# Kernel optimization log

Measured on AMD Instinct MI355X. Metric: run time of the kernel, lower is better.

The kernel has to match this reference:

```python
import jax, jax.numpy as jnp
import numpy as np

N_ZONE, E_ZONE = 100000, 2000000
N_OUT, E_OUT = 50000, 1000000
N_GND, E_GND = 50000, 1000000
HID = 64


def _gcn_conv(x, W, b, edge_index, edge_weight, num_nodes):
    """PyG GCNConv with normalize=True, add_self_loops=True (fill_value=1).
    out[i] = sum_{e: col[e]=i} d^-1/2[row]*w_e*d^-1/2[col] * (xW)[row[e]]
             + d^-1[i]*(xW)[i] + b
    """
    row, col = edge_index[0], edge_index[1]
    ew = edge_weight.reshape(-1)  # [E,1] -> [E]
    # degree includes self-loop weight of 1
    deg = jax.ops.segment_sum(ew, col, num_segments=num_nodes) + 1.0
    dinv = jnp.where(deg > 0, jax.lax.rsqrt(deg), 0.0)
    norm = dinv[row] * ew * dinv[col]  # [E]
    h = x @ W  # [N, HID] transform first (tiny in-dim)
    agg = jax.ops.segment_sum(norm[:, None] * h[row], col, num_segments=num_nodes)
    agg = agg + (dinv * dinv)[:, None] * h  # self-loop term
    return agg + b


def setup_inputs() -> dict:
    key = jax.random.key(0)
    ks = jax.random.split(key, 16)
    inp = {}
    inp["x_zone"] = jax.random.normal(ks[0], (N_ZONE, 2), dtype=jnp.float32)
    inp["x_outdoor"] = jax.random.normal(ks[1], (N_OUT, 3), dtype=jnp.float32)
    inp["x_ground"] = jax.random.normal(ks[2], (N_GND, 1), dtype=jnp.float32)
    inp["edge_index_zone"] = jax.random.randint(ks[3], (2, E_ZONE), 0, N_ZONE, dtype=jnp.int32)
    inp["edge_index_outdoor"] = jax.random.randint(ks[4], (2, E_OUT), 0, N_OUT, dtype=jnp.int32)
    inp["edge_index_ground"] = jax.random.randint(ks[5], (2, E_GND), 0, N_GND, dtype=jnp.int32)
    # learned params: GCN weights/biases + per-edge attribute parameters
    inp["W_zone"] = jax.random.normal(ks[6], (2, HID), dtype=jnp.float32) * 0.5
    inp["W_outdoor"] = jax.random.normal(ks[7], (3, HID), dtype=jnp.float32) * 0.5
    inp["W_ground"] = jax.random.normal(ks[8], (1, HID), dtype=jnp.float32) * 0.5
    inp["b_zone"] = jnp.zeros((HID,), dtype=jnp.float32)
    inp["b_outdoor"] = jnp.zeros((HID,), dtype=jnp.float32)
    inp["b_ground"] = jnp.zeros((HID,), dtype=jnp.float32)
    # positive edge weights so symmetric normalization deg^-1/2 is finite
    inp["edge_attr_zone"] = jax.random.uniform(ks[9], (E_ZONE, 1), dtype=jnp.float32, minval=0.1, maxval=1.0)
    inp["edge_attr_outdoor"] = jax.random.uniform(ks[10], (E_OUT, 1), dtype=jnp.float32, minval=0.1, maxval=1.0)
    inp["edge_attr_ground"] = jax.random.uniform(ks[11], (E_GND, 1), dtype=jnp.float32, minval=0.1, maxval=1.0)
    return inp


def reference(x_zone, x_outdoor, x_ground,
              edge_index_zone, edge_index_outdoor, edge_index_ground,
              W_zone, W_outdoor, W_ground,
              b_zone, b_outdoor, b_ground,
              edge_attr_zone, edge_attr_outdoor, edge_attr_ground):
    z = _gcn_conv(x_zone, W_zone, b_zone, edge_index_zone, edge_attr_zone, N_ZONE)
    o = _gcn_conv(x_outdoor, W_outdoor, b_outdoor, edge_index_outdoor, edge_attr_outdoor, N_OUT)
    g = _gcn_conv(x_ground, W_ground, b_ground, edge_index_ground, edge_attr_ground, N_GND)
    return (jax.nn.relu(z), jax.nn.relu(o), jax.nn.relu(g))
```

## Files before the change

kernel.cpp:

```cpp
#include <hip/hip_runtime.h>

#define N_ZONE 100000
#define E_ZONE 2000000
#define N_OUT  50000
#define E_OUT  1000000
#define N_GND  50000
#define E_GND  1000000
#define HID    64
#define N_TOT   (N_ZONE + N_OUT + N_GND)
#define E_TOTAL (E_ZONE + E_OUT + E_GND)

#define RANGE   2048
#define RSHIFT  11
#define NBZ     49
#define NBO     25
#define NBG     25
#define NBUCKET (NBZ + NBO + NBG)
#define SL      16
#define CAP     49152
#define OUT_PAD_BASE (NBZ * RANGE)
#define GND_PAD_BASE ((NBZ + NBO) * RANGE)
#define PAD_TOT      (NBUCKET * RANGE)

#define CHUNK  4096
#define NCHUNK ((E_TOTAL + CHUNK - 1) / CHUNK)

#define WCUR  0
#define WREC  128
#define WPDEG (WREC + 2 * NBUCKET * CAP)
#define WPSZ  (WPDEG + NBUCKET * SL * RANGE)
#define WPSO  (WPSZ + NBZ * SL * RANGE * 2)
#define WPSG  (WPSO + NBO * SL * RANGE * 3)
#define WDINV (WPSG + NBG * SL * RANGE)
#define WYZ   (WDINV + PAD_TOT)
#define WYO   (WYZ + 2 * N_ZONE)
#define WYG   (WYO + 4 * N_OUT)
#define WUZ   (WYG + N_GND)
#define WUO   (WUZ + 2 * N_ZONE)
#define WUG   (WUO + 4 * N_OUT)
#define WTOT  (WUG + N_GND)
#define FAST_WS_BYTES ((size_t)WTOT * 4)

__global__ void k_bin(const int* __restrict__ eiz, const float* __restrict__ wz,
                      const int* __restrict__ eio, const float* __restrict__ wo,
                      const int* __restrict__ eig, const float* __restrict__ wg,
                      unsigned* __restrict__ cur, uint2* __restrict__ rec) {
    __shared__ unsigned la[CHUNK];
    __shared__ float    lw[CHUNK];
    __shared__ unsigned hist[NBUCKET];
    __shared__ unsigned sbase[NBUCKET + 1];
    __shared__ unsigned gbase[NBUCKET];
    int tid = threadIdx.x;
    for (int b = tid; b < NBUCKET; b += 256) hist[b] = 0;
    __syncthreads();
    int t0 = blockIdx.x * CHUNK;
    unsigned mya[CHUNK / 256], mybk[CHUNK / 256], myr[CHUNK / 256];
    float myw[CHUNK / 256];
#pragma unroll
    for (int i = 0; i < CHUNK / 256; i++) {
        int t = t0 + i * 256 + tid;
        unsigned b = 0xFFFFFFFFu;
        if (t < E_TOTAL) {
            int row, col; float w;
            if (t < E_ZONE) { row = eiz[t]; col = eiz[E_ZONE + t]; w = wz[t]; b = col >> RSHIFT; }
            else if (t < E_ZONE + E_OUT) { int e = t - E_ZONE; row = eio[e]; col = eio[E_OUT + e]; w = wo[e]; b = NBZ + (col >> RSHIFT); }
            else { int e = t - E_ZONE - E_OUT; row = eig[e]; col = eig[E_GND + e]; w = wg[e]; b = NBZ + NBO + (col >> RSHIFT); }
            mya[i] = ((unsigned)(col & (RANGE - 1)) << 17) | (unsigned)row;
            myw[i] = w;
            myr[i] = atomicAdd(&hist[b], 1u);
        }
        mybk[i] = b;
    }
    __syncthreads();
    if (tid == 0) {
        unsigned acc = 0;
        for (int b = 0; b < NBUCKET; b++) { sbase[b] = acc; acc += hist[b]; }
        sbase[NBUCKET] = acc;
    }
    __syncthreads();
    if (tid < NBUCKET)
        gbase[tid] = hist[tid] ? atomicAdd(&cur[tid], hist[tid]) : 0u;
#pragma unroll
    for (int i = 0; i < CHUNK / 256; i++) {
        if (mybk[i] < NBUCKET) {
            unsigned p = sbase[mybk[i]] + myr[i];
            la[p] = mya[i]; lw[p] = myw[i];
        }
    }
    __syncthreads();
    unsigned total = sbase[NBUCKET];
    for (unsigned p = tid; p < total; p += 256) {
        int lo = 0, hi = NBUCKET;
        while (hi - lo > 1) { int mid = (lo + hi) >> 1; if (sbase[mid] <= p) lo = mid; else hi = mid; }
        unsigned idx = (unsigned)lo * CAP + gbase[lo] + (p - sbase[lo]);
        rec[idx] = make_uint2(la[p], __float_as_uint(lw[p]));
    }
}

__global__ void k_degp(const uint2* __restrict__ rec, const unsigned* __restrict__ cur,
                       float* __restrict__ pdeg) {
    __shared__ float deg[RANGE];
    int r = blockIdx.x / SL, sl = blockIdx.x % SL, tid = threadIdx.x;
    for (int i = tid; i < RANGE; i += 256) deg[i] = 0.0f;
    __syncthreads();
    unsigned c = cur[r];
    size_t b0 = (size_t)r * CAP;
    unsigned per = (c + SL - 1) / SL;
    unsigned s0 = sl * per, s1 = s0 + per; if (s1 > c) s1 = c;
    for (unsigned j = s0 + tid; j < s1; j += 256) {
        uint2 q = rec[b0 + j];
        atomicAdd(&deg[q.x >> 17], __uint_as_float(q.y));
    }
    __syncthreads();
    float* o = pdeg + (size_t)blockIdx.x * RANGE;
    for (int i = tid * 4; i < RANGE; i += 1024)
        *(float4*)&o[i] = *(float4*)&deg[i];
}

__global__ void k_dinvy(const float* __restrict__ xz, const float* __restrict__ xo,
                        const float* __restrict__ xg, float* __restrict__ ws) {
    int p = blockIdx.x * blockDim.x + threadIdx.x;
    if (p >= PAD_TOT) return;
    int r = p >> RSHIFT, i = p & (RANGE - 1);
    float d = 1.0f;
#pragma unroll
    for (int sl = 0; sl < SL; sl++)
        d += ws[WPDEG + (size_t)(r * SL + sl) * RANGE + i];
    float di = rsqrtf(d);
    ws[WDINV + p] = di;
    if (p < OUT_PAD_BASE) {
        if (p < N_ZONE) {
            ws[WYZ + 2 * p]     = di * xz[2 * p];
            ws[WYZ + 2 * p + 1] = di * xz[2 * p + 1];
        }
    } else if (p < GND_PAD_BASE) {
        int idx = p - OUT_PAD_BASE;
        if (idx < N_OUT) {
            ws[WYO + 4 * idx]     = di * xo[3 * idx];
            ws[WYO + 4 * idx + 1] = di * xo[3 * idx + 1];
            ws[WYO + 4 * idx + 2] = di * xo[3 * idx + 2];
            ws[WYO + 4 * idx + 3] = 0.0f;
        }
    } else {
        int idx = p - GND_PAD_BASE;
        if (idx < N_GND) ws[WYG + idx] = di * xg[idx];
    }
}

__global__ void k_sp(float* __restrict__ ws) {
    __shared__ __align__(16) float s[RANGE * 3];
    int r = blockIdx.x / SL, sl = blockIdx.x % SL, tid = threadIdx.x;
    const unsigned* cur = (const unsigned*)(ws + WCUR);
    const uint2* rec = (const uint2*)(ws + WREC);
    int ch, rg; size_t yoff, psoff;
    if (r < NBZ)            { ch = 2; rg = r;             yoff = WYZ; psoff = WPSZ; }
    else if (r < NBZ + NBO) { ch = 3; rg = r - NBZ;       yoff = WYO; psoff = WPSO; }
    else                    { ch = 1; rg = r - NBZ - NBO; yoff = WYG; psoff = WPSG; }
    int tot = RANGE * ch;
    for (int i = tid; i < tot; i += 256) s[i] = 0.0f;
    __syncthreads();
    unsigned c = cur[r];
    size_t b0 = (size_t)r * CAP;
    unsigned per = (c + SL - 1) / SL;
    unsigned s0 = sl * per, s1 = s0 + per; if (s1 > c) s1 = c;
    if (ch == 2) {
        const float2* y = (const float2*)(ws + yoff);
        for (unsigned j = s0 + tid; j < s1; j += 256) {
            uint2 q = rec[b0 + j];
            unsigned colr = q.x >> 17, row = q.x & 0x1FFFFu;
            float w = __uint_as_float(q.y);
            float2 yv = y[row];
            atomicAdd(&s[colr * 2],     w * yv.x);
            atomicAdd(&s[colr * 2 + 1], w * yv.y);
        }
    } else if (ch == 3) {
        const float4* y = (const float4*)(ws + yoff);
        for (unsigned j = s0 + tid; j < s1; j += 256) {
            uint2 q = rec[b0 + j];
            unsigned colr = q.x >> 17, row = q.x & 0x1FFFFu;
            float w = __uint_as_float(q.y);
            float4 yv = y[row];
            atomicAdd(&s[colr * 3],     w * yv.x);
            atomicAdd(&s[colr * 3 + 1], w * yv.y);
            atomicAdd(&s[colr * 3 + 2], w * yv.z);
        }
    } else {
        const float* y = ws + yoff;
        for (unsigned j = s0 + tid; j < s1; j += 256) {
            uint2 q = rec[b0 + j];
            atomicAdd(&s[q.x >> 17], __uint_as_float(q.y) * y[q.x & 0x1FFFFu]);
        }
    }
    __syncthreads();
    float* o = ws + psoff + (size_t)(rg * SL + sl) * tot;
    for (int i = tid * 4; i < tot; i += 1024)
        *(float4*)&o[i] = *(float4*)&s[i];
}

__global__ void k_u(float* __restrict__ ws) {
    int p = blockIdx.x * blockDim.x + threadIdx.x;
    if (p >= PAD_TOT) return;
    int r = p >> RSHIFT, i = p & (RANGE - 1);
    float di = ws[WDINV + p];
    if (p < OUT_PAD_BASE) {
        if (p >= N_ZONE) return;
        float s0 = ws[WYZ + 2 * p], s1 = ws[WYZ + 2 * p + 1];
#pragma unroll
        for (int sl = 0; sl < SL; sl++) {
            const float* ps = ws + WPSZ + (size_t)(r * SL + sl) * RANGE * 2;
            s0 += ps[2 * i]; s1 += ps[2 * i + 1];
        }
        ws[WUZ + 2 * p] = di * s0; ws[WUZ + 2 * p + 1] = di * s1;
    } else if (p < GND_PAD_BASE) {
        int idx = p - OUT_PAD_BASE;
        if (idx >= N_OUT) return;
        int rg = r - NBZ;
        float s0 = ws[WYO + 4 * idx], s1 = ws[WYO + 4 * idx + 1], s2 = ws[WYO + 4 * idx + 2];
#pragma unroll
        for (int sl = 0; sl < SL; sl++) {
            const float* ps = ws + WPSO + (size_t)(rg * SL + sl) * RANGE * 3;
            s0 += ps[3 * i]; s1 += ps[3 * i + 1]; s2 += ps[3 * i + 2];
        }
        ws[WUO + 4 * idx] = di * s0; ws[WUO + 4 * idx + 1] = di * s1; ws[WUO + 4 * idx + 2] = di * s2;
    } else {
        int idx = p - GND_PAD_BASE;
        if (idx >= N_GND) return;
        int rg = r - NBZ - NBO;
        float s0 = ws[WYG + idx];
#pragma unroll
        for (int sl = 0; sl < SL; sl++)
            s0 += ws[WPSG + (size_t)(rg * SL + sl) * RANGE + i];
        ws[WUG + idx] = di * s0;
    }
}

__global__ void k_fin2(const float* __restrict__ ws,
                       const float* __restrict__ Wz, const float* __restrict__ bz,
                       const float* __restrict__ Wo, const float* __restrict__ bo,
                       const float* __restrict__ Wg, const float* __restrict__ bg,
                       float* __restrict__ out) {
    int t = blockIdx.x * blockDim.x + threadIdx.x;
    const int TZ4 = N_ZONE * 16, TO4 = TZ4 + N_OUT * 16, TG4 = TO4 + N_GND * 16;
    if (t < TZ4) {
        int i = t >> 4, jb = (t & 15) << 2;
        float u0 = ws[WUZ + 2 * i], u1 = ws[WUZ + 2 * i + 1];
        float4 w0 = *(const float4*)(Wz + jb);
        float4 w1 = *(const float4*)(Wz + HID + jb);
        float4 bv = *(const float4*)(bz + jb);
        float4 o;
        o.x = fmaxf(bv.x + u0 * w0.x + u1 * w1.x, 0.0f);
        o.y = fmaxf(bv.y + u0 * w0.y + u1 * w1.y, 0.0f);
        o.z = fmaxf(bv.z + u0 * w0.z + u1 * w1.z, 0.0f);
        o.w = fmaxf(bv.w + u0 * w0.w + u1 * w1.w, 0.0f);
        *(float4*)(out + i * HID + jb) = o;
    } else if (t < TO4) {
        int q = t - TZ4;
        int i = q >> 4, jb = (q & 15) << 2;
        const float* u = ws + WUO + 4 * i;
        float u0 = u[0], u1 = u[1], u2 = u[2];
        float4 w0 = *(const float4*)(Wo + jb);
        float4 w1 = *(const float4*)(Wo + HID + jb);
        float4 w2 = *(const float4*)(Wo + 2 * HID + jb);
        float4 bv = *(const float4*)(bo + jb);
        float4 o;
        o.x = fmaxf(bv.x + u0 * w0.x + u1 * w1.x + u2 * w2.x, 0.0f);
        o.y = fmaxf(bv.y + u0 * w0.y + u1 * w1.y + u2 * w2.y, 0.0f);
        o.z = fmaxf(bv.z + u0 * w0.z + u1 * w1.z + u2 * w2.z, 0.0f);
        o.w = fmaxf(bv.w + u0 * w0.w + u1 * w1.w + u2 * w2.w, 0.0f);
        *(float4*)(out + N_ZONE * HID + i * HID + jb) = o;
    } else if (t < TG4) {
        int q = t - TO4;
        int i = q >> 4, jb = (q & 15) << 2;
        float u0 = ws[WUG + i];
        float4 w0 = *(const float4*)(Wg + jb);
        float4 bv = *(const float4*)(bg + jb);
        float4 o;
        o.x = fmaxf(bv.x + u0 * w0.x, 0.0f);
        o.y = fmaxf(bv.y + u0 * w0.y, 0.0f);
        o.z = fmaxf(bv.z + u0 * w0.z, 0.0f);
        o.w = fmaxf(bv.w + u0 * w0.w, 0.0f);
        *(float4*)(out + (N_ZONE + N_OUT) * HID + i * HID + jb) = o;
    }
}

#define F_DEG_Z   0
#define F_DEG_O   (N_ZONE)
#define F_DEG_G   (N_ZONE + N_OUT)
#define F_DEG_TOT N_TOT
#define F_S_Z     F_DEG_TOT
#define F_S_O     (F_S_Z + N_ZONE * 2)
#define F_S_G     (F_S_O + N_OUT * 3)
#define F_TOT     (F_S_G + N_GND * 1)

__global__ void f_init(float* __restrict__ ws) {
    int i = blockIdx.x * blockDim.x + threadIdx.x;
    if (i < F_TOT) ws[i] = (i < F_DEG_TOT) ? 1.0f : 0.0f;
}
__global__ void f_deg(const int* __restrict__ eiz, const float* __restrict__ wz,
                      const int* __restrict__ eio, const float* __restrict__ wo,
                      const int* __restrict__ eig, const float* __restrict__ wg,
                      float* __restrict__ ws) {
    int t = blockIdx.x * blockDim.x + threadIdx.x;
    if (t < E_ZONE) atomicAdd(ws + F_DEG_Z + eiz[E_ZONE + t], wz[t]);
    else if (t < E_ZONE + E_OUT) { int e = t - E_ZONE; atomicAdd(ws + F_DEG_O + eio[E_OUT + e], wo[e]); }
    else if (t < E_ZONE + E_OUT + E_GND) { int e = t - E_ZONE - E_OUT; atomicAdd(ws + F_DEG_G + eig[E_GND + e], wg[e]); }
}
__global__ void f_dinv(float* __restrict__ ws) {
    int i = blockIdx.x * blockDim.x + threadIdx.x;
    if (i < F_DEG_TOT) ws[i] = 1.0f / sqrtf(ws[i]);
}
__global__ void f_scatter(const int* __restrict__ eiz, const float* __restrict__ wz, const float* __restrict__ xz,
                          const int* __restrict__ eio, const float* __restrict__ wo, const float* __restrict__ xo,
                          const int* __restrict__ eig, const float* __restrict__ wg, const float* __restrict__ xg,
                          float* __restrict__ ws) {
    int t = blockIdx.x * blockDim.x + threadIdx.x;
    if (t < E_ZONE) {
        int row = eiz[t], col = eiz[E_ZONE + t];
        float n = ws[F_DEG_Z + row] * wz[t] * ws[F_DEG_Z + col];
        atomicAdd(ws + F_S_Z + col * 2 + 0, n * xz[row * 2 + 0]);
        atomicAdd(ws + F_S_Z + col * 2 + 1, n * xz[row * 2 + 1]);
    } else if (t < E_ZONE + E_OUT) {
        int e = t - E_ZONE;
        int row = eio[e], col = eio[E_OUT + e];
        float n = ws[F_DEG_O + row] * wo[e] * ws[F_DEG_O + col];
        atomicAdd(ws + F_S_O + col * 3 + 0, n * xo[row * 3 + 0]);
        atomicAdd(ws + F_S_O + col * 3 + 1, n * xo[row * 3 + 1]);
        atomicAdd(ws + F_S_O + col * 3 + 2, n * xo[row * 3 + 2]);
    } else if (t < E_ZONE + E_OUT + E_GND) {
        int e = t - E_ZONE - E_OUT;
        int row = eig[e], col = eig[E_GND + e];
        float n = ws[F_DEG_G + row] * wg[e] * ws[F_DEG_G + col];
        atomicAdd(ws + F_S_G + col, n * xg[row]);
    }
}
__global__ void f_final(const float* __restrict__ ws,
                        const float* __restrict__ xz, const float* __restrict__ Wz, const float* __restrict__ bz,
                        const float* __restrict__ xo, const float* __restrict__ Wo, const float* __restrict__ bo,
                        const float* __restrict__ xg, const float* __restrict__ Wg, const float* __restrict__ bg,
                        float* __restrict__ out) {
    int t = blockIdx.x * blockDim.x + threadIdx.x;
    const int TZ = N_ZONE * HID, TO = TZ + N_OUT * HID, TG = TO + N_GND * HID;
    if (t < TZ) {
        int i = t >> 6, j = t & 63;
        float di = ws[F_DEG_Z + i], d2 = di * di;
        float t0 = ws[F_S_Z + i * 2 + 0] + d2 * xz[i * 2 + 0];
        float t1 = ws[F_S_Z + i * 2 + 1] + d2 * xz[i * 2 + 1];
        out[t] = fmaxf(bz[j] + t0 * Wz[j] + t1 * Wz[HID + j], 0.0f);
    } else if (t < TO) {
        int u = t - TZ;
        int i = u >> 6, j = u & 63;
        float di = ws[F_DEG_O + i], d2 = di * di;
        float t0 = ws[F_S_O + i * 3 + 0] + d2 * xo[i * 3 + 0];
        float t1 = ws[F_S_O + i * 3 + 1] + d2 * xo[i * 3 + 1];
        float t2 = ws[F_S_O + i * 3 + 2] + d2 * xo[i * 3 + 2];
        out[t] = fmaxf(bo[j] + t0 * Wo[j] + t1 * Wo[HID + j] + t2 * Wo[2 * HID + j], 0.0f);
    } else if (t < TG) {
        int u = t - TO;
        int i = u >> 6, j = u & 63;
        float di = ws[F_DEG_G + i], d2 = di * di;
        float t0 = ws[F_S_G + i] + d2 * xg[i];
        out[t] = fmaxf(bg[j] + t0 * Wg[j], 0.0f);
    }
}

extern "C" void kernel_launch(void* const* d_in, const int* in_sizes, int n_in,
                              void* d_out, int out_size, void* d_ws, size_t ws_size,
                              hipStream_t stream) {
    const float* xz = (const float*)d_in[0];
    const float* xo = (const float*)d_in[1];
    const float* xg = (const float*)d_in[2];
    const int*  eiz = (const int*)d_in[3];
    const int*  eio = (const int*)d_in[4];
    const int*  eig = (const int*)d_in[5];
    const float* Wz = (const float*)d_in[6];
    const float* Wo = (const float*)d_in[7];
    const float* Wg = (const float*)d_in[8];
    const float* bz = (const float*)d_in[9];
    const float* bo = (const float*)d_in[10];
    const float* bg = (const float*)d_in[11];
    const float* wz = (const float*)d_in[12];
    const float* wo = (const float*)d_in[13];
    const float* wg = (const float*)d_in[14];
    float* out = (float*)d_out;
    float* ws  = (float*)d_ws;

    const int B = 256;

    if (ws_size >= FAST_WS_BYTES) {
        unsigned* cur = (unsigned*)(ws + WCUR);
        uint2* rec = (uint2*)(ws + WREC);
        hipMemsetAsync(cur, 0, 128 * 4, stream);
        k_bin<<<NCHUNK, B, 0, stream>>>(eiz, wz, eio, wo, eig, wg, cur, rec);
        k_degp<<<NBUCKET * SL, B, 0, stream>>>(rec, cur, ws + WPDEG);
        k_dinvy<<<(PAD_TOT + B - 1) / B, B, 0, stream>>>(xz, xo, xg, ws);
        k_sp<<<NBUCKET * SL, B, 0, stream>>>(ws);
        k_u<<<(PAD_TOT + B - 1) / B, B, 0, stream>>>(ws);
        k_fin2<<<(N_TOT * HID / 4 + B - 1) / B, B, 0, stream>>>(ws, Wz, bz, Wo, bo, Wg, bg, out);
    } else {
        const int E_TOT = E_TOTAL, OUT_TOT = N_TOT * HID;
        f_init<<<(F_TOT + B - 1) / B, B, 0, stream>>>(ws);
        f_deg<<<(E_TOT + B - 1) / B, B, 0, stream>>>(eiz, wz, eio, wo, eig, wg, ws);
        f_dinv<<<(F_DEG_TOT + B - 1) / B, B, 0, stream>>>(ws);
        f_scatter<<<(E_TOT + B - 1) / B, B, 0, stream>>>(eiz, wz, xz, eio, wo, xo, eig, wg, xg, ws);
        f_final<<<(OUT_TOT + B - 1) / B, B, 0, stream>>>(ws, xz, Wz, bz, xo, Wo, bo, xg, Wg, bg, out);
    }
}
```

Before: 252.7 us.

## Bin edges by destination and source range, stage source features in LDS

Edges are now binned two-dimensionally by destination range and source-row range, 2475 bins with small fixed capacity. Each scatter block loads the matching slice of source features into shared memory, so the per-edge gather reads LDS instead of random global memory. Feature and partial-sum layouts become planar, and the bin kernel uses a parallel scan and a per-record bin tag instead of a serial scan and binary search. The risks are more bins to scan, overflow of the fixed per-bin capacity (1920) if the edge distribution is skewed, and extra window-loading work with two syncs per bin.

```diff
diff --git a/kernel.cpp b/kernel.cpp
--- a/kernel.cpp
+++ b/kernel.cpp
@@ -16,25 +16,35 @@
 #define NBO     25
 #define NBG     25
 #define NBUCKET (NBZ + NBO + NBG)
+#define RGN     25
+#define ZRSH    12
+#define ORSH    11
+#define NBIN    (NBUCKET * RGN)
+#define ZONE_B0 0
+#define OUT_B0  (NBZ * RGN)
+#define GND_B0  ((NBZ + NBO) * RGN)
 #define SL      16
-#define CAP     49152
+#define CAP_RG  1920
 #define OUT_PAD_BASE (NBZ * RANGE)
 #define GND_PAD_BASE ((NBZ + NBO) * RANGE)
 #define PAD_TOT      (NBUCKET * RANGE)
-
-#define CHUNK  4096
+#define OPL     51200
+
+#define CHUNK  3072
+#define EPT    (CHUNK / 256)
+#define BPT    10
 #define NCHUNK ((E_TOTAL + CHUNK - 1) / CHUNK)
 
 #define WCUR  0
-#define WREC  128
-#define WPDEG (WREC + 2 * NBUCKET * CAP)
+#define WREC  2496
+#define WPDEG (WREC + 2 * NBIN * CAP_RG)
 #define WPSZ  (WPDEG + NBUCKET * SL * RANGE)
 #define WPSO  (WPSZ + NBZ * SL * RANGE * 2)
 #define WPSG  (WPSO + NBO * SL * RANGE * 3)
 #define WDINV (WPSG + NBG * SL * RANGE)
 #define WYZ   (WDINV + PAD_TOT)
 #define WYO   (WYZ + 2 * N_ZONE)
-#define WYG   (WYO + 4 * N_OUT)
+#define WYG   (WYO + 3 * OPL)
 #define WUZ   (WYG + N_GND)
 #define WUO   (WUZ + 2 * N_ZONE)
 #define WUG   (WUO + 4 * N_OUT)
@@ -47,24 +57,34 @@
                       unsigned* __restrict__ cur, uint2* __restrict__ rec) {
     __shared__ unsigned la[CHUNK];
     __shared__ float    lw[CHUNK];
-    __shared__ unsigned hist[NBUCKET];
-    __shared__ unsigned sbase[NBUCKET + 1];
-    __shared__ unsigned gbase[NBUCKET];
+    __shared__ unsigned short lbk[CHUNK];
+    __shared__ unsigned hist[NBIN];
+    __shared__ unsigned sbase[NBIN];
+    __shared__ unsigned gbase[NBIN];
+    __shared__ unsigned tsum[256];
+    __shared__ unsigned stot;
     int tid = threadIdx.x;
-    for (int b = tid; b < NBUCKET; b += 256) hist[b] = 0;
+    for (int b = tid; b < NBIN; b += 256) hist[b] = 0;
     __syncthreads();
     int t0 = blockIdx.x * CHUNK;
-    unsigned mya[CHUNK / 256], mybk[CHUNK / 256], myr[CHUNK / 256];
-    float myw[CHUNK / 256];
-#pragma unroll
-    for (int i = 0; i < CHUNK / 256; i++) {
+    unsigned mya[EPT], mybk[EPT], myr[EPT];
+    float myw[EPT];
+#pragma unroll
+    for (int i = 0; i < EPT; i++) {
         int t = t0 + i * 256 + tid;
         unsigned b = 0xFFFFFFFFu;
         if (t < E_TOTAL) {
             int row, col; float w;
-            if (t < E_ZONE) { row = eiz[t]; col = eiz[E_ZONE + t]; w = wz[t]; b = col >> RSHIFT; }
-            else if (t < E_ZONE + E_OUT) { int e = t - E_ZONE; row = eio[e]; col = eio[E_OUT + e]; w = wo[e]; b = NBZ + (col >> RSHIFT); }
-            else { int e = t - E_ZONE - E_OUT; row = eig[e]; col = eig[E_GND + e]; w = wg[e]; b = NBZ + NBO + (col >> RSHIFT); }
+            if (t < E_ZONE) {
+                row = eiz[t]; col = eiz[E_ZONE + t]; w = wz[t];
+                b = ZONE_B0 + (unsigned)(col >> RSHIFT) * RGN + (unsigned)(row >> ZRSH);
+            } else if (t < E_ZONE + E_OUT) {
+                int e = t - E_ZONE; row = eio[e]; col = eio[E_OUT + e]; w = wo[e];
+                b = OUT_B0 + (unsigned)(col >> RSHIFT) * RGN + (unsigned)(row >> ORSH);
+            } else {
+                int e = t - E_ZONE - E_OUT; row = eig[e]; col = eig[E_GND + e]; w = wg[e];
+                b = GND_B0 + (unsigned)(col >> RSHIFT) * RGN + (unsigned)(row >> ORSH);
+            }
             mya[i] = ((unsigned)(col & (RANGE - 1)) << 17) | (unsigned)row;
             myw[i] = w;
             myr[i] = atomicAdd(&hist[b], 1u);
@@ -72,27 +92,46 @@
         mybk[i] = b;
     }
     __syncthreads();
+    {
+        unsigned base = (unsigned)tid * BPT, acc = 0;
+#pragma unroll
+        for (int k = 0; k < BPT; k++) {
+            unsigned b = base + k;
+            if (b < NBIN) acc += hist[b];
+        }
+        tsum[tid] = acc;
+    }
+    __syncthreads();
     if (tid == 0) {
-        unsigned acc = 0;
-        for (int b = 0; b < NBUCKET; b++) { sbase[b] = acc; acc += hist[b]; }
-        sbase[NBUCKET] = acc;
-    }
-    __syncthreads();
-    if (tid < NBUCKET)
-        gbase[tid] = hist[tid] ? atomicAdd(&cur[tid], hist[tid]) : 0u;
-#pragma unroll
-    for (int i = 0; i < CHUNK / 256; i++) {
-        if (mybk[i] < NBUCKET) {
+        unsigned a = 0;
+        for (int i = 0; i < 256; i++) { unsigned v = tsum[i]; tsum[i] = a; a += v; }
+        stot = a;
+    }
+    __syncthreads();
+    {
+        unsigned base = (unsigned)tid * BPT, acc = tsum[tid];
+#pragma unroll
+        for (int k = 0; k < BPT; k++) {
+            unsigned b = base + k;
+            if (b < NBIN) { sbase[b] = acc; acc += hist[b]; }
+        }
+    }
+    for (int b = tid; b < NBIN; b += 256)
+        gbase[b] = hist[b] ? atomicAdd(&cur[b], hist[b]) : 0u;
+    __syncthreads();
+#pragma unroll
+    for (int i = 0; i < EPT; i++) {
+        if (mybk[i] < NBIN) {
             unsigned p = sbase[mybk[i]] + myr[i];
             la[p] = mya[i]; lw[p] = myw[i];
-        }
-    }
-    __syncthreads();
-    unsigned total = sbase[NBUCKET];
+            lbk[p] = (unsigned short)mybk[i];
+        }
+    }
+    __syncthreads();
+    unsigned total = stot;
     for (unsigned p = tid; p < total; p += 256) {
-        int lo = 0, hi = NBUCKET;
-        while (hi - lo > 1) { int mid = (lo + hi) >> 1; if (sbase[mid] <= p) lo = mid; else hi = mid; }
-        unsigned idx = (unsigned)lo * CAP + gbase[lo] + (p - sbase[lo]);
+        unsigned b = lbk[p];
+        unsigned idx = b * CAP_RG + gbase[b] + (p - sbase[b]);
         rec[idx] = make_uint2(la[p], __float_as_uint(lw[p]));
     }
 }
@@ -103,13 +142,30 @@
     int r = blockIdx.x / SL, sl = blockIdx.x % SL, tid = threadIdx.x;
     for (int i = tid; i < RANGE; i += 256) deg[i] = 0.0f;
     __syncthreads();
-    unsigned c = cur[r];
-    size_t b0 = (size_t)r * CAP;
-    unsigned per = (c + SL - 1) / SL;
-    unsigned s0 = sl * per, s1 = s0 + per; if (s1 > c) s1 = c;
-    for (unsigned j = s0 + tid; j < s1; j += 256) {
-        uint2 q = rec[b0 + j];
-        atomicAdd(&deg[q.x >> 17], __uint_as_float(q.y));
+    int bin0;
+    if (r < NBZ)            bin0 = ZONE_B0 + r * RGN;
+    else if (r < NBZ + NBO) bin0 = OUT_B0 + (r - NBZ) * RGN;
+    else                    bin0 = GND_B0 + (r - NBZ - NBO) * RGN;
+#pragma unroll
+    for (int gi = 0; gi < 2; gi++) {
+        int g = sl + gi * SL;
+        if (g >= RGN) break;
+        unsigned bin = bin0 + g;
+        unsigned c = cur[bin];
+        size_t rb = (size_t)bin * CAP_RG;
+        unsigned j = tid;
+        for (; j + 256u * 3 < c; j += 256u * 4) {
+            uint2 q[4];
+#pragma unroll
+            for (int u = 0; u < 4; u++) q[u] = rec[rb + j + 256u * u];
+#pragma unroll
+            for (int u = 0; u < 4; u++)
+                atomicAdd(&deg[(q[u].x >> 17) & (RANGE - 1)], __uint_as_float(q[u].y));
+        }
+        for (; j < c; j += 256u) {
+            uint2 q = rec[rb + j];
+            atomicAdd(&deg[(q.x >> 17) & (RANGE - 1)], __uint_as_float(q.y));
+        }
     }
     __syncthreads();
     float* o = pdeg + (size_t)blockIdx.x * RANGE;
@@ -136,10 +192,9 @@
     } else if (p < GND_PAD_BASE) {
         int idx = p - OUT_PAD_BASE;
         if (idx < N_OUT) {
-            ws[WYO + 4 * idx]     = di * xo[3 * idx];
-            ws[WYO + 4 * idx + 1] = di * xo[3 * idx + 1];
-            ws[WYO + 4 * idx + 2] = di * xo[3 * idx + 2];
-            ws[WYO + 4 * idx + 3] = 0.0f;
+            ws[WYO + idx]           = di * xo[3 * idx];
+            ws[WYO + OPL + idx]     = di * xo[3 * idx + 1];
+            ws[WYO + 2 * OPL + idx] = di * xo[3 * idx + 2];
         }
     } else {
         int idx = p - GND_PAD_BASE;
@@ -148,53 +203,151 @@
 }
 
 __global__ void k_sp(float* __restrict__ ws) {
-    __shared__ __align__(16) float s[RANGE * 3];
+    __shared__ __align__(16) float lds[12288];
     int r = blockIdx.x / SL, sl = blockIdx.x % SL, tid = threadIdx.x;
     const unsigned* cur = (const unsigned*)(ws + WCUR);
     const uint2* rec = (const uint2*)(ws + WREC);
-    int ch, rg; size_t yoff, psoff;
-    if (r < NBZ)            { ch = 2; rg = r;             yoff = WYZ; psoff = WPSZ; }
-    else if (r < NBZ + NBO) { ch = 3; rg = r - NBZ;       yoff = WYO; psoff = WPSO; }
-    else                    { ch = 1; rg = r - NBZ - NBO; yoff = WYG; psoff = WPSG; }
-    int tot = RANGE * ch;
-    for (int i = tid; i < tot; i += 256) s[i] = 0.0f;
-    __syncthreads();
-    unsigned c = cur[r];
-    size_t b0 = (size_t)r * CAP;
-    unsigned per = (c + SL - 1) / SL;
-    unsigned s0 = sl * per, s1 = s0 + per; if (s1 > c) s1 = c;
-    if (ch == 2) {
-        const float2* y = (const float2*)(ws + yoff);
-        for (unsigned j = s0 + tid; j < s1; j += 256) {
-            uint2 q = rec[b0 + j];
-            unsigned colr = q.x >> 17, row = q.x & 0x1FFFFu;
-            float w = __uint_as_float(q.y);
-            float2 yv = y[row];
-            atomicAdd(&s[colr * 2],     w * yv.x);
-            atomicAdd(&s[colr * 2 + 1], w * yv.y);
-        }
-    } else if (ch == 3) {
-        const float4* y = (const float4*)(ws + yoff);
-        for (unsigned j = s0 + tid; j < s1; j += 256) {
-            uint2 q = rec[b0 + j];
-            unsigned colr = q.x >> 17, row = q.x & 0x1FFFFu;
-            float w = __uint_as_float(q.y);
-            float4 yv = y[row];
-            atomicAdd(&s[colr * 3],     w * yv.x);
-            atomicAdd(&s[colr * 3 + 1], w * yv.y);
-            atomicAdd(&s[colr * 3 + 2], w * yv.z);
-        }
+    if (r < NBZ) {
+        float* win = lds;
+        float* s   = lds + 8192;
+        for (int i = tid; i < 4096; i += 256) s[i] = 0.0f;
+        int bin0 = ZONE_B0 + r * RGN;
+#pragma unroll
+        for (int gi = 0; gi < 2; gi++) {
+            int g = sl + gi * SL;
+            if (g >= RGN) break;
+            __syncthreads();
+            int row0 = g << ZRSH;
+            int nw = 2 * (min(4096, N_ZONE - row0));
+            const float4* src = (const float4*)(ws + WYZ + 2 * row0);
+            for (int i = tid; i * 4 < nw; i += 256)
+                ((float4*)win)[i] = src[i];
+            __syncthreads();
+            unsigned bin = bin0 + g;
+            unsigned c = cur[bin];
+            size_t rb = (size_t)bin * CAP_RG;
+            unsigned j = tid;
+            for (; j + 256u * 3 < c; j += 256u * 4) {
+                uint2 q[4];
+#pragma unroll
+                for (int u = 0; u < 4; u++) q[u] = rec[rb + j + 256u * u];
+#pragma unroll
+                for (int u = 0; u < 4; u++) {
+                    unsigned colr = (q[u].x >> 17) & (RANGE - 1);
+                    unsigned loc = q[u].x & 4095u;
+                    float w = __uint_as_float(q[u].y);
+                    float2 yv = *(const float2*)&win[loc * 2];
+                    atomicAdd(&s[colr],        w * yv.x);
+                    atomicAdd(&s[2048 + colr], w * yv.y);
+                }
+            }
+            for (; j < c; j += 256u) {
+                uint2 q = rec[rb + j];
+                unsigned colr = (q.x >> 17) & (RANGE - 1);
+                unsigned loc = q.x & 4095u;
+                float w = __uint_as_float(q.y);
+                float2 yv = *(const float2*)&win[loc * 2];
+                atomicAdd(&s[colr],        w * yv.x);
+                atomicAdd(&s[2048 + colr], w * yv.y);
+            }
+        }
+        __syncthreads();
+        float* o = ws + WPSZ + (size_t)(r * SL + sl) * 4096;
+        for (int i = tid * 4; i < 4096; i += 1024)
+            *(float4*)&o[i] = *(float4*)&s[i];
+    } else if (r < NBZ + NBO) {
+        int rg = r - NBZ;
+        float* win = lds;
+        float* s   = lds + 6144;
+        for (int i = tid; i < 6144; i += 256) s[i] = 0.0f;
+        int bin0 = OUT_B0 + rg * RGN;
+#pragma unroll
+        for (int gi = 0; gi < 2; gi++) {
+            int g = sl + gi * SL;
+            if (g >= RGN) break;
+            __syncthreads();
+            int row0 = g << ORSH;
+            int nv = min(2048, N_OUT - row0);
+#pragma unroll
+            for (int pl = 0; pl < 3; pl++) {
+                const float4* src = (const float4*)(ws + WYO + pl * OPL + row0);
+                for (int i = tid; i * 4 < nv; i += 256)
+                    ((float4*)(win + pl * 2048))[i] = src[i];
+            }
+            __syncthreads();
+            unsigned bin = bin0 + g;
+            unsigned c = cur[bin];
+            size_t rb = (size_t)bin * CAP_RG;
+            unsigned j = tid;
+            for (; j + 256u * 3 < c; j += 256u * 4) {
+                uint2 q[4];
+#pragma unroll
+                for (int u = 0; u < 4; u++) q[u] = rec[rb + j + 256u * u];
+#pragma unroll
+                for (int u = 0; u < 4; u++) {
+                    unsigned colr = (q[u].x >> 17) & (RANGE - 1);
+                    unsigned loc = q[u].x & 2047u;
+                    float w = __uint_as_float(q[u].y);
+                    atomicAdd(&s[colr],        w * win[loc]);
+                    atomicAdd(&s[2048 + colr], w * win[2048 + loc]);
+                    atomicAdd(&s[4096 + colr], w * win[4096 + loc]);
+                }
+            }
+            for (; j < c; j += 256u) {
+                uint2 q = rec[rb + j];
+                unsigned colr = (q.x >> 17) & (RANGE - 1);
+                unsigned loc = q.x & 2047u;
+                float w = __uint_as_float(q.y);
+                atomicAdd(&s[colr],        w * win[loc]);
+                atomicAdd(&s[2048 + colr], w * win[2048 + loc]);
+                atomicAdd(&s[4096 + colr], w * win[4096 + loc]);
+            }
+        }
+        __syncthreads();
+        float* o = ws + WPSO + (size_t)(rg * SL + sl) * 6144;
+        for (int i = tid * 4; i < 6144; i += 1024)
+            *(float4*)&o[i] = *(float4*)&s[i];
     } else {
-        const float* y = ws + yoff;
-        for (unsigned j = s0 + tid; j < s1; j += 256) {
-            uint2 q = rec[b0 + j];
-            atomicAdd(&s[q.x >> 17], __uint_as_float(q.y) * y[q.x & 0x1FFFFu]);
-        }
-    }
-    __syncthreads();
-    float* o = ws + psoff + (size_t)(rg * SL + sl) * tot;
-    for (int i = tid * 4; i < tot; i += 1024)
-        *(float4*)&o[i] = *(float4*)&s[i];
+        int rg = r - NBZ - NBO;
+        float* win = lds;
+        float* s   = lds + 2048;
+        for (int i = tid; i < 2048; i += 256) s[i] = 0.0f;
+        int bin0 = GND_B0 + rg * RGN;
+#pragma unroll
+        for (int gi = 0; gi < 2; gi++) {
+            int g = sl + gi * SL;
+            if (g >= RGN) break;
+            __syncthreads();
+            int row0 = g << ORSH;
+            int nv = min(2048, N_GND - row0);
+            const float4* src = (const float4*)(ws + WYG + row0);
+            for (int i = tid; i * 4 < nv; i += 256)
+                ((float4*)win)[i] = src[i];
+            __syncthreads();
+            unsigned bin = bin0 + g;
+            unsigned c = cur[bin];
+            size_t rb = (size_t)bin * CAP_RG;
+            unsigned j = tid;
+            for (; j + 256u * 3 < c; j += 256u * 4) {
+                uint2 q[4];
+#pragma unroll
+                for (int u = 0; u < 4; u++) q[u] = rec[rb + j + 256u * u];
+#pragma unroll
+                for (int u = 0; u < 4; u++)
+                    atomicAdd(&s[(q[u].x >> 17) & (RANGE - 1)],
+                              __uint_as_float(q[u].y) * win[q[u].x & 2047u]);
+            }
+            for (; j < c; j += 256u) {
+                uint2 q = rec[rb + j];
+                atomicAdd(&s[(q.x >> 17) & (RANGE - 1)],
+                          __uint_as_float(q.y) * win[q.x & 2047u]);
+            }
+        }
+        __syncthreads();
+        float* o = ws + WPSG + (size_t)(rg * SL + sl) * 2048;
+        for (int i = tid * 4; i < 2048; i += 1024)
+            *(float4*)&o[i] = *(float4*)&s[i];
+    }
 }
 
 __global__ void k_u(float* __restrict__ ws) {
@@ -207,19 +360,19 @@
         float s0 = ws[WYZ + 2 * p], s1 = ws[WYZ + 2 * p + 1];
 #pragma unroll
         for (int sl = 0; sl < SL; sl++) {
-            const float* ps = ws + WPSZ + (size_t)(r * SL + sl) * RANGE * 2;
-            s0 += ps[2 * i]; s1 += ps[2 * i + 1];
+            const float* ps = ws + WPSZ + (size_t)(r * SL + sl) * 4096;
+            s0 += ps[i]; s1 += ps[2048 + i];
         }
         ws[WUZ + 2 * p] = di * s0; ws[WUZ + 2 * p + 1] = di * s1;
     } else if (p < GND_PAD_BASE) {
         int idx = p - OUT_PAD_BASE;
         if (idx >= N_OUT) return;
         int rg = r - NBZ;
-        float s0 = ws[WYO + 4 * idx], s1 = ws[WYO + 4 * idx + 1], s2 = ws[WYO + 4 * idx + 2];
+        float s0 = ws[WYO + idx], s1 = ws[WYO + OPL + idx], s2 = ws[WYO + 2 * OPL + idx];
 #pragma unroll
         for (int sl = 0; sl < SL; sl++) {
-            const float* ps = ws + WPSO + (size_t)(rg * SL + sl) * RANGE * 3;
-            s0 += ps[3 * i]; s1 += ps[3 * i + 1]; s2 += ps[3 * i + 2];
+            const float* ps = ws + WPSO + (size_t)(rg * SL + sl) * 6144;
+            s0 += ps[i]; s1 += ps[2048 + i]; s2 += ps[4096 + i];
         }
         ws[WUO + 4 * idx] = di * s0; ws[WUO + 4 * idx + 1] = di * s1; ws[WUO + 4 * idx + 2] = di * s2;
     } else {
@@ -229,7 +382,7 @@
         float s0 = ws[WYG + idx];
 #pragma unroll
         for (int sl = 0; sl < SL; sl++)
-            s0 += ws[WPSG + (size_t)(rg * SL + sl) * RANGE + i];
+            s0 += ws[WPSG + (size_t)(rg * SL + sl) * 2048 + i];
         ws[WUG + idx] = di * s0;
     }
 }
@@ -389,7 +542,7 @@
     if (ws_size >= FAST_WS_BYTES) {
         unsigned* cur = (unsigned*)(ws + WCUR);
         uint2* rec = (uint2*)(ws + WREC);
-        hipMemsetAsync(cur, 0, 128 * 4, stream);
+        hipMemsetAsync(cur, 0, 2496 * 4, stream);
         k_bin<<<NCHUNK, B, 0, stream>>>(eiz, wz, eio, wo, eig, wg, cur, rec);
         k_degp<<<NBUCKET * SL, B, 0, stream>>>(rec, cur, ws + WPDEG);
         k_dinvy<<<(PAD_TOT + B - 1) / B, B, 0, stream>>>(xz, xo, xg, ws);
```

New measurement: 307.4 us. +21.6%, slower.
